# Kernel tuning notes

Measured on AMD Instinct MI355X. Metric: run time of the kernel, lower is better.

The kernel has to match this reference:

```python
import jax, jax.numpy as jnp
import numpy as np


def _unpack_i4(packed):
    """Unpack int8 bytes into two signed int4 values (low nibble first),
    matching quarot.functional.pack_i4's interleaved layout."""
    p = packed.astype(jnp.int8)
    low = jnp.right_shift(jnp.left_shift(p, 4), 4)   # sign-extended low nibble
    high = jnp.right_shift(p, 4)                      # arithmetic shift -> signed high nibble
    return jnp.stack([low, high], axis=-1).reshape(*p.shape[:-1], p.shape[-1] * 2)


def setup_inputs() -> dict:
    key = jax.random.key(0)
    k1, k2, k3, k4 = jax.random.split(key, 4)
    M, K, N = 4096, 4096, 11008
    # packed int4 activations / weights: each byte holds two signed 4-bit values
    x_q = jax.random.randint(k1, (M, K // 2), 0, 256, dtype=jnp.int32)
    weight = jax.random.randint(k3, (N, K // 2), 0, 256, dtype=jnp.int32)
    # per-row dequant scales (small positive values, as real quant scales are)
    scales_x = (jax.random.uniform(k2, (M, 1), dtype=jnp.float32) * 0.01 + 1e-3).astype(jnp.float16)
    weight_scales = (jax.random.uniform(k4, (N,), dtype=jnp.float32) * 0.01 + 1e-3).astype(jnp.float16)
    return {"x_q": x_q, "scales_x": scales_x, "weight": weight, "weight_scales": weight_scales}


def reference(x_q, scales_x, weight, weight_scales):
    # Unpack int4 -> exact small integers; fp32 matmul accumulates them exactly
    # (|sum| <= 8*8*4096 < 2^24), emulating quarot.fuse_matmul's int4 GEMM.
    A = _unpack_i4(x_q).astype(jnp.float32)      # [M, K]
    B = _unpack_i4(weight).astype(jnp.float32)   # [N, K]
    acc = jnp.einsum('mk,nk->mn', A, B)          # [M, N] integer-exact GEMM
    # fused per-row (activation) x per-channel (weight) dequantization
    out = acc * scales_x.astype(jnp.float32) * weight_scales.astype(jnp.float32)[None, :]
    return out.astype(jnp.float16)
```

## Files before the change

### kernel.cpp

```cpp
#include <hip/hip_runtime.h>

typedef int v4i __attribute__((ext_vector_type(4)));

#define M_DIM 4096
#define N_DIM 11008
#define K_DIM 4096
#define KP    (K_DIM / 2)
#define NSLAB (K_DIM / 64)

__device__ __forceinline__ unsigned pack2(int p) {
    int lo = (p << 28) >> 28;
    int hi = (p << 24) >> 28;
    return (unsigned)(lo & 0xFF) | ((unsigned)(hi & 0xFF) << 8);
}

__device__ __forceinline__ void unpack_group(int4 p, unsigned &slo, unsigned &shi) {
    unsigned c = ((unsigned)p.x & 0xFFu)
               | (((unsigned)p.y & 0xFFu) << 8)
               | (((unsigned)p.z & 0xFFu) << 16)
               | (((unsigned)p.w & 0xFFu) << 24);
    slo = (c & 0x0F0F0F0Fu) | ((c & 0x08080808u) * 30u);
    unsigned d = c >> 4;
    shi = (d & 0x0F0F0F0Fu) | ((d & 0x08080808u) * 30u);
}

__global__ __launch_bounds__(256) void unpack_i4_all(
    const int* __restrict__ inA, const int* __restrict__ inB,
    uint2* __restrict__ out, int n4A, int n4tot)
{
    int idx = blockIdx.x * blockDim.x + threadIdx.x;
    if (idx >= n4tot) return;
    int4 v;
    if (idx < n4A) v = ((const int4*)inA)[idx];
    else           v = ((const int4*)inB)[idx - n4A];
    unsigned d0 = pack2(v.x) | (pack2(v.y) << 16);
    unsigned d1 = pack2(v.z) | (pack2(v.w) << 16);
    out[idx] = make_uint2(d0, d1);
}

__global__ __launch_bounds__(256, 2) void gemm_i8_kernel(
    const unsigned char* __restrict__ A8, const unsigned char* __restrict__ B8,
    const float* __restrict__ sx, const float* __restrict__ sw,
    float* __restrict__ out)
{
    __shared__ v4i smem[4096];
    unsigned char* smemAll = (unsigned char*)smem;

    const int t    = threadIdx.x;
    const int lane = t & 63;
    const int w    = t >> 6;
    const int wm   = w >> 1;
    const int wn   = w & 1;
    const int rowBase = blockIdx.y * 128;
    const int colBase = blockIdx.x * 128;

    const int c0 = t, c1 = t + 256;
    const int r0 = (c0 >> 6) * 16 + (c0 & 15);
    const int r1 = (c1 >> 6) * 16 + (c1 & 15);
    const int q0 = (c0 >> 4) & 3;
    const int q1 = (c1 >> 4) & 3;

    const unsigned char* gA0 = A8 + (size_t)(rowBase + r0) * K_DIM + q0 * 16;
    const unsigned char* gA1 = A8 + (size_t)(rowBase + r1) * K_DIM + q1 * 16;
    const unsigned char* gB0 = B8 + (size_t)(colBase + r0) * K_DIM + q0 * 16;
    const unsigned char* gB1 = B8 + (size_t)(colBase + r1) * K_DIM + q1 * 16;

    const int oA0 = c0 * 16;
    const int oA1 = c1 * 16;
    const int oB0 = 8192 + c0 * 16;
    const int oB1 = 8192 + c1 * 16;

    v4i acc[4][4] = {};

#define STAGE(S) do {                                                          \
    unsigned char* _b = smemAll + (((S) & 3) << 14);                           \
    const int _kb = (S) * 64;                                                  \
    __builtin_amdgcn_global_load_lds(                                          \
        (const __attribute__((address_space(1))) void*)(gA0 + _kb),            \
        (__attribute__((address_space(3))) void*)(_b + oA0), 16, 0, 0);        \
    __builtin_amdgcn_global_load_lds(                                          \
        (const __attribute__((address_space(1))) void*)(gA1 + _kb),            \
        (__attribute__((address_space(3))) void*)(_b + oA1), 16, 0, 0);        \
    __builtin_amdgcn_global_load_lds(                                          \
        (const __attribute__((address_space(1))) void*)(gB0 + _kb),            \
        (__attribute__((address_space(3))) void*)(_b + oB0), 16, 0, 0);        \
    __builtin_amdgcn_global_load_lds(                                          \
        (const __attribute__((address_space(1))) void*)(gB1 + _kb),            \
        (__attribute__((address_space(3))) void*)(_b + oB1), 16, 0, 0);        \
} while (0)

#define COMPUTE(S) do {                                                        \
    const unsigned char* _b = smemAll + (((S) & 3) << 14);                     \
    v4i af[4], bf[4];                                                          \
    _Pragma("unroll")                                                          \
    for (int mt = 0; mt < 4; ++mt)                                             \
        af[mt] = *((const v4i*)(_b + (((wm * 4 + mt) * 64 + lane) << 4)));     \
    _Pragma("unroll")                                                          \
    for (int nt = 0; nt < 4; ++nt)                                             \
        bf[nt] = *((const v4i*)(_b + 8192 + (((wn * 4 + nt) * 64 + lane) << 4))); \
    __builtin_amdgcn_s_setprio(1);                                             \
    _Pragma("unroll")                                                          \
    for (int mt = 0; mt < 4; ++mt)                                             \
        _Pragma("unroll")                                                      \
        for (int nt = 0; nt < 4; ++nt)                                         \
            acc[mt][nt] = __builtin_amdgcn_mfma_i32_16x16x64_i8(               \
                af[mt], bf[nt], acc[mt][nt], 0, 0, 0);                         \
    __builtin_amdgcn_s_setprio(0);                                             \
} while (0)

    STAGE(0); STAGE(1); STAGE(2);

    for (int s = 0; s < NSLAB - 3; ++s) {
        asm volatile("s_waitcnt vmcnt(8)" ::: "memory");
        __builtin_amdgcn_s_barrier();
        __builtin_amdgcn_sched_barrier(0);
        STAGE(s + 3);
        COMPUTE(s);
    }
    asm volatile("s_waitcnt vmcnt(8)" ::: "memory");
    __builtin_amdgcn_s_barrier();
    __builtin_amdgcn_sched_barrier(0);
    COMPUTE(NSLAB - 3);
    asm volatile("s_waitcnt vmcnt(4)" ::: "memory");
    __builtin_amdgcn_s_barrier();
    __builtin_amdgcn_sched_barrier(0);
    COMPUTE(NSLAB - 2);
    asm volatile("s_waitcnt vmcnt(0)" ::: "memory");
    __builtin_amdgcn_s_barrier();
    __builtin_amdgcn_sched_barrier(0);
    COMPUTE(NSLAB - 1);

#undef STAGE
#undef COMPUTE

    const int ccol = lane & 15;
    const int crow = (lane >> 4) * 4;

    float xs[4][4];
    #pragma unroll
    for (int mt = 0; mt < 4; ++mt)
        #pragma unroll
        for (int r = 0; r < 4; ++r)
            xs[mt][r] = sx[rowBase + wm * 64 + mt * 16 + crow + r];

    #pragma unroll
    for (int nt = 0; nt < 4; ++nt) {
        const int gn = colBase + wn * 64 + nt * 16 + ccol;
        const float wsc = sw[gn];
        #pragma unroll
        for (int mt = 0; mt < 4; ++mt) {
            const int gm = rowBase + wm * 64 + mt * 16 + crow;
            #pragma unroll
            for (int r = 0; r < 4; ++r) {
                float v = (float)acc[mt][nt][r] * xs[mt][r] * wsc;
                out[(size_t)(gm + r) * N_DIM + gn] = v;
            }
        }
    }
}

__global__ __launch_bounds__(256) void gemm_i4_fused_kernel(
    const int* __restrict__ Aq, const int* __restrict__ Bq,
    const float* __restrict__ sx, const float* __restrict__ sw,
    float* __restrict__ out)
{
    __shared__ v4i smem[1024];
    unsigned char* smemA = (unsigned char*)smem;
    unsigned char* smemB = smemA + 8192;

    const int t    = threadIdx.x;
    const int lane = t & 63;
    const int w    = t >> 6;
    const int wm   = w >> 1;
    const int wn   = w & 1;
    const int rowBase = blockIdx.y * 128;
    const int colBase = blockIdx.x * 128;

    const int c0 = t, c1 = t + 256;
    const int r0 = (c0 >> 6) * 16 + (c0 & 15);
    const int r1 = (c1 >> 6) * 16 + (c1 & 15);
    const int q0 = (c0 >> 4) & 3;
    const int q1 = (c1 >> 4) & 3;

    const int* gA0 = Aq + (size_t)(rowBase + r0) * KP + q0 * 8;
    const int* gA1 = Aq + (size_t)(rowBase + r1) * KP + q1 * 8;
    const int* gB0 = Bq + (size_t)(colBase + r0) * KP + q0 * 8;
    const int* gB1 = Bq + (size_t)(colBase + r1) * KP + q1 * 8;

    v4i* lA0 = (v4i*)(smemA + c0 * 16);
    v4i* lA1 = (v4i*)(smemA + c1 * 16);
    v4i* lB0 = (v4i*)(smemB + c0 * 16);
    v4i* lB1 = (v4i*)(smemB + c1 * 16);

    v4i acc[4][4] = {};

    for (int kb = 0; kb < K_DIM; kb += 64) {
        const int kp = kb >> 1;
        int4 a00 = *(const int4*)(gA0 + kp);
        int4 a01 = *(const int4*)(gA0 + kp + 4);
        int4 a10 = *(const int4*)(gA1 + kp);
        int4 a11 = *(const int4*)(gA1 + kp + 4);
        int4 b00 = *(const int4*)(gB0 + kp);
        int4 b01 = *(const int4*)(gB0 + kp + 4);
        int4 b10 = *(const int4*)(gB1 + kp);
        int4 b11 = *(const int4*)(gB1 + kp + 4);

        __syncthreads();

        unsigned u0, u1, u2, u3;
        unpack_group(a00, u0, u1); unpack_group(a01, u2, u3);
        *lA0 = (v4i){(int)u0, (int)u1, (int)u2, (int)u3};
        unpack_group(a10, u0, u1); unpack_group(a11, u2, u3);
        *lA1 = (v4i){(int)u0, (int)u1, (int)u2, (int)u3};
        unpack_group(b00, u0, u1); unpack_group(b01, u2, u3);
        *lB0 = (v4i){(int)u0, (int)u1, (int)u2, (int)u3};
        unpack_group(b10, u0, u1); unpack_group(b11, u2, u3);
        *lB1 = (v4i){(int)u0, (int)u1, (int)u2, (int)u3};

        __syncthreads();

        v4i af[4], bf[4];
        #pragma unroll
        for (int mt = 0; mt < 4; ++mt)
            af[mt] = *((const v4i*)(smemA + ((wm * 4 + mt) * 64 + lane) * 16));
        #pragma unroll
        for (int nt = 0; nt < 4; ++nt)
            bf[nt] = *((const v4i*)(smemB + ((wn * 4 + nt) * 64 + lane) * 16));

        #pragma unroll
        for (int mt = 0; mt < 4; ++mt)
            #pragma unroll
            for (int nt = 0; nt < 4; ++nt)
                acc[mt][nt] = __builtin_amdgcn_mfma_i32_16x16x64_i8(
                    af[mt], bf[nt], acc[mt][nt], 0, 0, 0);
    }

    const int ccol = lane & 15;
    const int crow = (lane >> 4) * 4;

    float xs[4][4];
    #pragma unroll
    for (int mt = 0; mt < 4; ++mt)
        #pragma unroll
        for (int r = 0; r < 4; ++r)
            xs[mt][r] = sx[rowBase + wm * 64 + mt * 16 + crow + r];

    #pragma unroll
    for (int nt = 0; nt < 4; ++nt) {
        const int gn = colBase + wn * 64 + nt * 16 + ccol;
        const float wsc = sw[gn];
        #pragma unroll
        for (int mt = 0; mt < 4; ++mt) {
            const int gm = rowBase + wm * 64 + mt * 16 + crow;
            #pragma unroll
            for (int r = 0; r < 4; ++r) {
                float v = (float)acc[mt][nt][r] * xs[mt][r] * wsc;
                out[(size_t)(gm + r) * N_DIM + gn] = v;
            }
        }
    }
}

extern "C" void kernel_launch(void* const* d_in, const int* in_sizes, int n_in,
                              void* d_out, int out_size, void* d_ws, size_t ws_size,
                              hipStream_t stream) {
    (void)in_sizes; (void)n_in; (void)out_size;
    const int*   x_q = (const int*)d_in[0];
    const float* sx  = (const float*)d_in[1];
    const int*   w_q = (const int*)d_in[2];
    const float* sw  = (const float*)d_in[3];
    float*       out = (float*)d_out;

    dim3 grid(N_DIM / 128, M_DIM / 128);

    const size_t needA = (size_t)M_DIM * K_DIM;
    const size_t needB = (size_t)N_DIM * K_DIM;
    if (ws_size >= needA + needB) {
        unsigned char* A8 = (unsigned char*)d_ws;
        unsigned char* B8 = A8 + needA;
        const int n4A = M_DIM * KP / 4;
        const int n4B = N_DIM * KP / 4;
        const int n4T = n4A + n4B;
        unpack_i4_all<<<n4T / 256, 256, 0, stream>>>(x_q, w_q, (uint2*)d_ws, n4A, n4T);
        gemm_i8_kernel<<<grid, 256, 0, stream>>>(A8, B8, sx, sw, out);
    } else {
        gemm_i4_fused_kernel<<<grid, 256, 0, stream>>>(x_q, w_q, sx, sw, out);
    }
}
```

Before: 584.3 us.

## Enlarge int8 GEMM tile to 256x256 with XCD-aware block remap

The int8 MFMA GEMM moves from 128x128 tiles with 4 waves to 256x256 tiles with 8 waves (512 threads). Each wave now computes an 8x4 grid of 16x16 fragments, and the LDS ring grows to four 32KB stages. Global-to-LDS prefetch of the next stage is split into A and B halves and interleaved between the two MFMA groups. A 1D grid with a modulo-8 block remap groups neighbouring tiles per XCD for L2 reuse, and the unpack kernel becomes a grid-stride loop with a fixed block count. Larger tiles cut global and LDS traffic per MFMA, but occupancy drops to one large block per CU and the tile count leaves a wave-quantization tail.

After: 487.3 us. 16.6% less time.

```diff
diff --git a/kernel.cpp b/kernel.cpp
--- a/kernel.cpp
+++ b/kernel.cpp
@@ -6,7 +6,7 @@
 #define N_DIM 11008
 #define K_DIM 4096
 #define KP    (K_DIM / 2)
-#define NSLAB (K_DIM / 64)
+#define NKT   (K_DIM / 64)
 
 __device__ __forceinline__ unsigned pack2(int p) {
     int lo = (p << 28) >> 28;
@@ -28,52 +28,58 @@
     const int* __restrict__ inA, const int* __restrict__ inB,
     uint2* __restrict__ out, int n4A, int n4tot)
 {
-    int idx = blockIdx.x * blockDim.x + threadIdx.x;
-    if (idx >= n4tot) return;
-    int4 v;
-    if (idx < n4A) v = ((const int4*)inA)[idx];
-    else           v = ((const int4*)inB)[idx - n4A];
-    unsigned d0 = pack2(v.x) | (pack2(v.y) << 16);
-    unsigned d1 = pack2(v.z) | (pack2(v.w) << 16);
-    out[idx] = make_uint2(d0, d1);
-}
-
-__global__ __launch_bounds__(256, 2) void gemm_i8_kernel(
+    for (int idx = blockIdx.x * blockDim.x + threadIdx.x; idx < n4tot;
+         idx += gridDim.x * blockDim.x) {
+        int4 v;
+        if (idx < n4A) v = ((const int4*)inA)[idx];
+        else           v = ((const int4*)inB)[idx - n4A];
+        unsigned d0 = pack2(v.x) | (pack2(v.y) << 16);
+        unsigned d1 = pack2(v.z) | (pack2(v.w) << 16);
+        out[idx] = make_uint2(d0, d1);
+    }
+}
+
+__global__ __launch_bounds__(512, 2) void gemm_i8_kernel(
     const unsigned char* __restrict__ A8, const unsigned char* __restrict__ B8,
     const float* __restrict__ sx, const float* __restrict__ sw,
     float* __restrict__ out)
 {
-    __shared__ v4i smem[4096];
+    __shared__ v4i smem[8192];
     unsigned char* smemAll = (unsigned char*)smem;
 
     const int t    = threadIdx.x;
     const int lane = t & 63;
     const int w    = t >> 6;
-    const int wm   = w >> 1;
-    const int wn   = w & 1;
-    const int rowBase = blockIdx.y * 128;
-    const int colBase = blockIdx.x * 128;
-
-    const int c0 = t, c1 = t + 256;
-    const int r0 = (c0 >> 6) * 16 + (c0 & 15);
-    const int r1 = (c1 >> 6) * 16 + (c1 & 15);
-    const int q0 = (c0 >> 4) & 3;
-    const int q1 = (c1 >> 4) & 3;
-
-    const unsigned char* gA0 = A8 + (size_t)(rowBase + r0) * K_DIM + q0 * 16;
-    const unsigned char* gA1 = A8 + (size_t)(rowBase + r1) * K_DIM + q1 * 16;
-    const unsigned char* gB0 = B8 + (size_t)(colBase + r0) * K_DIM + q0 * 16;
-    const unsigned char* gB1 = B8 + (size_t)(colBase + r1) * K_DIM + q1 * 16;
-
-    const int oA0 = c0 * 16;
-    const int oA1 = c1 * 16;
-    const int oB0 = 8192 + c0 * 16;
-    const int oB1 = 8192 + c1 * 16;
-
-    v4i acc[4][4] = {};
-
-#define STAGE(S) do {                                                          \
-    unsigned char* _b = smemAll + (((S) & 3) << 14);                           \
+    const int wm   = w >> 2;
+    const int wn   = w & 3;
+
+    const int orig = blockIdx.x;
+    const int wgid = (orig & 7) * 86 + (orig >> 3);
+    const int bx   = wgid >> 4;
+    const int by   = wgid & 15;
+    const int rowBase = by * 256;
+    const int colBase = bx * 256;
+
+    const int cA0 = t, cA1 = t + 512;
+    const int rA0 = (cA0 >> 6) * 16 + (cA0 & 15);
+    const int rA1 = (cA1 >> 6) * 16 + (cA1 & 15);
+    const int qA0 = ((cA0 >> 4) & 3) * 16;
+    const int qA1 = ((cA1 >> 4) & 3) * 16;
+
+    const unsigned char* gA0 = A8 + (size_t)(rowBase + rA0) * K_DIM + qA0;
+    const unsigned char* gA1 = A8 + (size_t)(rowBase + rA1) * K_DIM + qA1;
+    const unsigned char* gB0 = B8 + (size_t)(colBase + rA0) * K_DIM + qA0;
+    const unsigned char* gB1 = B8 + (size_t)(colBase + rA1) * K_DIM + qA1;
+
+    const int oA0 = cA0 * 16;
+    const int oA1 = cA1 * 16;
+    const int oB0 = 16384 + cA0 * 16;
+    const int oB1 = 16384 + cA1 * 16;
+
+    v4i acc[8][4] = {};
+
+#define STAGE_A(S) do {                                                        \
+    unsigned char* _b = smemAll + (((S) & 3) << 15);                           \
     const int _kb = (S) * 64;                                                  \
     __builtin_amdgcn_global_load_lds(                                          \
         (const __attribute__((address_space(1))) void*)(gA0 + _kb),            \
@@ -81,6 +87,11 @@
     __builtin_amdgcn_global_load_lds(                                          \
         (const __attribute__((address_space(1))) void*)(gA1 + _kb),            \
         (__attribute__((address_space(3))) void*)(_b + oA1), 16, 0, 0);        \
+} while (0)
+
+#define STAGE_B(S) do {                                                        \
+    unsigned char* _b = smemAll + (((S) & 3) << 15);                           \
+    const int _kb = (S) * 64;                                                  \
     __builtin_amdgcn_global_load_lds(                                          \
         (const __attribute__((address_space(1))) void*)(gB0 + _kb),            \
         (__attribute__((address_space(3))) void*)(_b + oB0), 16, 0, 0);        \
@@ -89,67 +100,84 @@
         (__attribute__((address_space(3))) void*)(_b + oB1), 16, 0, 0);        \
 } while (0)
 
-#define COMPUTE(S) do {                                                        \
-    const unsigned char* _b = smemAll + (((S) & 3) << 14);                     \
-    v4i af[4], bf[4];                                                          \
+#define COMPUTE(S, DO_STAGE, SS) do {                                          \
+    const unsigned char* _b = smemAll + (((S) & 3) << 15);                     \
+    v4i bf[4];                                                                 \
+    _Pragma("unroll")                                                          \
+    for (int nt = 0; nt < 4; ++nt)                                             \
+        bf[nt] = *((const v4i*)(_b + 16384 + (((wn * 4 + nt) * 64 + lane) << 4))); \
+    v4i af0[4];                                                                \
     _Pragma("unroll")                                                          \
     for (int mt = 0; mt < 4; ++mt)                                             \
-        af[mt] = *((const v4i*)(_b + (((wm * 4 + mt) * 64 + lane) << 4)));     \
-    _Pragma("unroll")                                                          \
-    for (int nt = 0; nt < 4; ++nt)                                             \
-        bf[nt] = *((const v4i*)(_b + 8192 + (((wn * 4 + nt) * 64 + lane) << 4))); \
+        af0[mt] = *((const v4i*)(_b + (((wm * 8 + mt) * 64 + lane) << 4)));    \
+    if (DO_STAGE) STAGE_A(SS);                                                 \
     __builtin_amdgcn_s_setprio(1);                                             \
     _Pragma("unroll")                                                          \
     for (int mt = 0; mt < 4; ++mt)                                             \
         _Pragma("unroll")                                                      \
         for (int nt = 0; nt < 4; ++nt)                                         \
             acc[mt][nt] = __builtin_amdgcn_mfma_i32_16x16x64_i8(               \
-                af[mt], bf[nt], acc[mt][nt], 0, 0, 0);                         \
+                af0[mt], bf[nt], acc[mt][nt], 0, 0, 0);                        \
+    __builtin_amdgcn_s_setprio(0);                                             \
+    v4i af1[4];                                                                \
+    _Pragma("unroll")                                                          \
+    for (int mt = 0; mt < 4; ++mt)                                             \
+        af1[mt] = *((const v4i*)(_b + (((wm * 8 + 4 + mt) * 64 + lane) << 4))); \
+    if (DO_STAGE) STAGE_B(SS);                                                 \
+    __builtin_amdgcn_s_setprio(1);                                             \
+    _Pragma("unroll")                                                          \
+    for (int mt = 0; mt < 4; ++mt)                                             \
+        _Pragma("unroll")                                                      \
+        for (int nt = 0; nt < 4; ++nt)                                         \
+            acc[4 + mt][nt] = __builtin_amdgcn_mfma_i32_16x16x64_i8(           \
+                af1[mt], bf[nt], acc[4 + mt][nt], 0, 0, 0);                    \
     __builtin_amdgcn_s_setprio(0);                                             \
 } while (0)
 
-    STAGE(0); STAGE(1); STAGE(2);
-
-    for (int s = 0; s < NSLAB - 3; ++s) {
+    STAGE_A(0); STAGE_B(0);
+    STAGE_A(1); STAGE_B(1);
+    STAGE_A(2); STAGE_B(2);
+
+    for (int kt = 0; kt < NKT - 3; ++kt) {
         asm volatile("s_waitcnt vmcnt(8)" ::: "memory");
         __builtin_amdgcn_s_barrier();
         __builtin_amdgcn_sched_barrier(0);
-        STAGE(s + 3);
-        COMPUTE(s);
+        COMPUTE(kt, 1, kt + 3);
     }
     asm volatile("s_waitcnt vmcnt(8)" ::: "memory");
     __builtin_amdgcn_s_barrier();
     __builtin_amdgcn_sched_barrier(0);
-    COMPUTE(NSLAB - 3);
+    COMPUTE(NKT - 3, 0, 0);
     asm volatile("s_waitcnt vmcnt(4)" ::: "memory");
     __builtin_amdgcn_s_barrier();
     __builtin_amdgcn_sched_barrier(0);
-    COMPUTE(NSLAB - 2);
+    COMPUTE(NKT - 2, 0, 0);
     asm volatile("s_waitcnt vmcnt(0)" ::: "memory");
     __builtin_amdgcn_s_barrier();
     __builtin_amdgcn_sched_barrier(0);
-    COMPUTE(NSLAB - 1);
-
-#undef STAGE
+    COMPUTE(NKT - 1, 0, 0);
+
+#undef STAGE_A
+#undef STAGE_B
 #undef COMPUTE
 
     const int ccol = lane & 15;
     const int crow = (lane >> 4) * 4;
 
-    float xs[4][4];
+    float xs[8][4];
     #pragma unroll
-    for (int mt = 0; mt < 4; ++mt)
+    for (int mt = 0; mt < 8; ++mt)
         #pragma unroll
         for (int r = 0; r < 4; ++r)
-            xs[mt][r] = sx[rowBase + wm * 64 + mt * 16 + crow + r];
+            xs[mt][r] = sx[rowBase + wm * 128 + mt * 16 + crow + r];
 
     #pragma unroll
     for (int nt = 0; nt < 4; ++nt) {
         const int gn = colBase + wn * 64 + nt * 16 + ccol;
         const float wsc = sw[gn];
         #pragma unroll
-        for (int mt = 0; mt < 4; ++mt) {
-            const int gm = rowBase + wm * 64 + mt * 16 + crow;
+        for (int mt = 0; mt < 8; ++mt) {
+            const int gm = rowBase + wm * 128 + mt * 16 + crow;
             #pragma unroll
             for (int r = 0; r < 4; ++r) {
                 float v = (float)acc[mt][nt][r] * xs[mt][r] * wsc;
@@ -271,8 +299,6 @@
     const float* sw  = (const float*)d_in[3];
     float*       out = (float*)d_out;
 
-    dim3 grid(N_DIM / 128, M_DIM / 128);
-
     const size_t needA = (size_t)M_DIM * K_DIM;
     const size_t needB = (size_t)N_DIM * K_DIM;
     if (ws_size >= needA + needB) {
@@ -281,9 +307,10 @@
         const int n4A = M_DIM * KP / 4;
         const int n4B = N_DIM * KP / 4;
         const int n4T = n4A + n4B;
-        unpack_i4_all<<<n4T / 256, 256, 0, stream>>>(x_q, w_q, (uint2*)d_ws, n4A, n4T);
-        gemm_i8_kernel<<<grid, 256, 0, stream>>>(A8, B8, sx, sw, out);
+        unpack_i4_all<<<2048, 256, 0, stream>>>(x_q, w_q, (uint2*)d_ws, n4A, n4T);
+        gemm_i8_kernel<<<688, 512, 0, stream>>>(A8, B8, sx, sw, out);
     } else {
+        dim3 grid(N_DIM / 128, M_DIM / 128);
         gemm_i4_fused_kernel<<<grid, 256, 0, stream>>>(x_q, w_q, sx, sw, out);
     }
 }
```
